# Kernel optimization log

Hardware: AMD Instinct MI355X
Metric: run time of the kernel (lower is better)

## Reference

```python
import jax, jax.numpy as jnp
import numpy as np
import math

# ---- static configuration (matches init_kwargs) ----
METADATA = [64, 48, 32]   # channels per l = 0,1,2
MAX_L = 3                 # order_out
N_BATCH = 32768
fact = math.factorial

def _cg_complex(l1, m1, l2, m2, l3, m3):
    # Clebsch-Gordan coefficient <l1 m1 l2 m2 | l3 m3> via Racah formula
    if m1 + m2 != m3 or l3 < abs(l1 - l2) or l3 > l1 + l2:
        return 0.0
    pre = math.sqrt((2*l3+1) * fact(l1+l2-l3) * fact(l1-l2+l3) * fact(-l1+l2+l3) / fact(l1+l2+l3+1))
    pre *= math.sqrt(fact(l1+m1)*fact(l1-m1)*fact(l2+m2)*fact(l2-m2)*fact(l3+m3)*fact(l3-m3))
    kmin = max(0, l2-l3-m1, l1-l3+m2)
    kmax = min(l1+l2-l3, l1-m1, l2+m2)
    s = 0.0
    for k in range(kmin, kmax+1):
        s += (-1)**k / (fact(k)*fact(l1+l2-l3-k)*fact(l1-m1-k)*fact(l2+m2-k)*fact(l3-l2+m1+k)*fact(l3-l1-m2+k))
    return pre * s

def _U(l):
    # complex->real spherical harmonic change of basis, rows = real m', cols = complex m
    U = np.zeros((2*l+1, 2*l+1), dtype=np.complex128)
    for m in range(-l, l+1):
        r = m + l
        if m > 0:
            U[r, m+l] = (-1)**m / math.sqrt(2.0); U[r, -m+l] = 1.0/math.sqrt(2.0)
        elif m == 0:
            U[r, l] = 1.0
        else:
            U[r, m+l] = 1j/math.sqrt(2.0); U[r, -m+l] = -1j*(-1)**m/math.sqrt(2.0)
    return U

def _real_cg(l1, l2, l3):
    Cc = np.zeros((2*l1+1, 2*l2+1, 2*l3+1))
    for m1 in range(-l1, l1+1):
        for m2 in range(-l2, l2+1):
            for m3 in range(-l3, l3+1):
                Cc[m1+l1, m2+l2, m3+l3] = _cg_complex(l1, m1, l2, m2, l3, m3)
    T = np.einsum('am,bn,co,mno->abc', _U(l1), _U(l2), _U(l3).conj(), Cc.astype(np.complex128))
    T = T.imag if np.abs(T.imag).max() > np.abs(T.real).max() else T.real
    return np.ascontiguousarray(T).astype(np.float32)

# ---- static index structures ----
L_IN = len(METADATA)
OFF_IN = np.concatenate([[0], np.cumsum([METADATA[l]*(2*l+1) for l in range(L_IN)])]).astype(np.int64)
DIM_IN = int(OFF_IN[-1])  # 368
PATHS = []
for l1 in range(L_IN):
    for l2 in range(L_IN):
        for l3 in range(abs(l1-l2), min(l1+l2, MAX_L)+1):
            PATHS.append((l1, l2, l3, min(METADATA[l1], METADATA[l2])))
MD_OV = [0]*(MAX_L+1)
for (_, _, l3, ch) in PATHS:
    MD_OV[l3] = max(MD_OV[l3], ch)
OFF_OUT = np.concatenate([[0], np.cumsum([MD_OV[l]*(2*l+1) for l in range(MAX_L+1)])]).astype(np.int64)
DIM_OUT = int(OFF_OUT[-1])  # 672
CG = {(l1, l2, l3): jnp.asarray(_real_cg(l1, l2, l3)) for (l1, l2, l3, _) in PATHS}

_mix_id, _scat = [], []
_base = 0
for (l1, l2, l3, ch) in PATHS:
    for i in range(ch):
        for m in range(2*l3+1):
            _mix_id.append(_base + i)
            _scat.append(int(OFF_OUT[l3]) + i*(2*l3+1) + m)
    _base += ch
MIX_ID = jnp.asarray(np.array(_mix_id, dtype=np.int64))
SCATTER = jnp.asarray(np.array(_scat, dtype=np.int64))
N_MIX = _base  # 688

_chan_in = []
_cb = 0
for l in range(L_IN):
    for i in range(METADATA[l]):
        _chan_in += [_cb + i]*(2*l+1)
    _cb += METADATA[l]
CHAN_IN = jnp.asarray(np.array(_chan_in, dtype=np.int64))
N_KEEP = _cb  # 144
_kin, _kout = [], []
for l in range(L_IN):
    cp = min(METADATA[l], MD_OV[l])
    for i in range(cp):
        for m in range(2*l+1):
            _kin.append(int(OFF_IN[l]) + i*(2*l+1) + m)
            _kout.append(int(OFF_OUT[l]) + i*(2*l+1) + m)
KEEP_IN = jnp.asarray(np.array(_kin, dtype=np.int64))
KEEP_OUT = jnp.asarray(np.array(_kout, dtype=np.int64))

SQ3 = math.sqrt(3.0)

def setup_inputs() -> dict:
    key = jax.random.key(0)
    k1, k2, k3 = jax.random.split(key, 3)
    x = jax.random.normal(k1, (N_BATCH, DIM_IN), dtype=jnp.float32)
    keep_coeff = jax.random.uniform(k2, (N_KEEP,), minval=-SQ3, maxval=SQ3, dtype=jnp.float32)
    mix_coeff = jax.random.uniform(k3, (N_MIX,), minval=-SQ3, maxval=SQ3, dtype=jnp.float32)
    return {"x": x, "keep_coeff": keep_coeff, "mix_coeff": mix_coeff}

def reference(x, keep_coeff, mix_coeff):
    n = x.shape[0]
    # keep path: per-channel coeff broadcast over m components
    x_keep = x * keep_coeff[CHAN_IN]  # [N, 368]
    # CG tensor-product self-coupling (diagonal channel pairing per path)
    tps = []
    for (l1, l2, l3, ch) in PATHS:
        x1 = x[:, OFF_IN[l1]:OFF_IN[l1]+ch*(2*l1+1)].reshape(n, ch, 2*l1+1)
        x2 = x[:, OFF_IN[l2]:OFF_IN[l2]+ch*(2*l2+1)].reshape(n, ch, 2*l2+1)
        tps.append(jnp.einsum('nia,nib,abm->nim', x1, x2, CG[(l1, l2, l3)]).reshape(n, -1))
    cat = jnp.concatenate(tps, axis=1)  # [N, 2576] non-overlapped TP output
    cat = cat * 0.5 * mix_coeff[MIX_ID]
    # scatter (index_add) into overlapped output layout
    out = jnp.zeros((n, DIM_OUT), dtype=x.dtype).at[:, SCATTER].add(cat)
    # gather + add of keep path (index_select + add_)
    out = out.at[:, KEEP_OUT].add(x_keep[:, KEEP_IN])
    return out
```

## Files before the change

kernel.cpp:

```cpp
#include <hip/hip_runtime.h>


namespace cgc {

struct cplx { double re, im; };
constexpr cplx cmul(cplx a, cplx b){ return {a.re*b.re - a.im*b.im, a.re*b.im + a.im*b.re}; }

constexpr double cfact(int n){ double r = 1.0; for (int i = 2; i <= n; ++i) r *= i; return r; }
constexpr double cabsd(double x){ return x < 0 ? -x : x; }

constexpr double csqrtd(double x){
  if (x <= 0.0) return 0.0;
  double g = x > 1.0 ? x : 1.0;
  for (int i = 0; i < 48; ++i) g = 0.5*(g + x/g);
  return g;
}

constexpr double SQRT2 = csqrtd(2.0);

constexpr double cg_complex(int l1,int m1,int l2,int m2,int l3,int m3){
  if (m1 + m2 != m3) return 0.0;
  int lo = l1 > l2 ? l1 - l2 : l2 - l1;
  if (l3 < lo || l3 > l1 + l2) return 0.0;
  double pre = csqrtd((2*l3+1) * cfact(l1+l2-l3)*cfact(l1-l2+l3)*cfact(-l1+l2+l3)/cfact(l1+l2+l3+1));
  pre *= csqrtd(cfact(l1+m1)*cfact(l1-m1)*cfact(l2+m2)*cfact(l2-m2)*cfact(l3+m3)*cfact(l3-m3));
  int kmin = 0;
  if (l2-l3-m1 > kmin) kmin = l2-l3-m1;
  if (l1-l3+m2 > kmin) kmin = l1-l3+m2;
  int kmax = l1+l2-l3;
  if (l1-m1 < kmax) kmax = l1-m1;
  if (l2+m2 < kmax) kmax = l2+m2;
  double s = 0.0;
  for (int k = kmin; k <= kmax; ++k){
    double d = cfact(k)*cfact(l1+l2-l3-k)*cfact(l1-m1-k)*cfact(l2+m2-k)
             * cfact(l3-l2+m1+k)*cfact(l3-l1-m2+k);
    s += ((k & 1) ? -1.0 : 1.0) / d;
  }
  return pre * s;
}

constexpr cplx Uent(int l, int r, int c){
  int m = r - l;
  if (m > 0){
    if (c ==  m + l) return { ((m & 1) ? -1.0 : 1.0)/SQRT2, 0.0 };
    if (c == -m + l) return { 1.0/SQRT2, 0.0 };
    return {0.0, 0.0};
  } else if (m == 0){
    if (c == l) return {1.0, 0.0};
    return {0.0, 0.0};
  } else {
    int ma = -m;
    if (c ==  m + l) return { 0.0, 1.0/SQRT2 };
    if (c == -m + l) return { 0.0, -(((ma & 1) ? -1.0 : 1.0))/SQRT2 };
    return {0.0, 0.0};
  }
}

template<int L1,int L2,int L3>
struct CGData { float w[(2*L1+1)*(2*L2+1)*(2*L3+1)]; };

template<int L1,int L2,int L3>
constexpr CGData<L1,L2,L3> make_cg(){
  constexpr int D1 = 2*L1+1, D2 = 2*L2+1, D3 = 2*L3+1;
  cplx U1[D1*D1] = {}; cplx U2[D2*D2] = {}; cplx U3c[D3*D3] = {};
  for (int r = 0; r < D1; ++r) for (int c = 0; c < D1; ++c) U1[r*D1+c] = Uent(L1, r, c);
  for (int r = 0; r < D2; ++r) for (int c = 0; c < D2; ++c) U2[r*D2+c] = Uent(L2, r, c);
  for (int r = 0; r < D3; ++r) for (int c = 0; c < D3; ++c){
    cplx u = Uent(L3, r, c); u.im = -u.im; U3c[r*D3+c] = u;
  }
  double Cc[D1*D2*D3] = {};
  for (int m1 = -L1; m1 <= L1; ++m1)
    for (int m2 = -L2; m2 <= L2; ++m2){
      int m3 = m1 + m2;
      if (m3 < -L3 || m3 > L3) continue;
      Cc[((m1+L1)*D2 + (m2+L2))*D3 + (m3+L3)] = cg_complex(L1,m1,L2,m2,L3,m3);
    }
  double re[D1*D2*D3] = {}; double im[D1*D2*D3] = {};
  for (int a = 0; a < D1; ++a)
    for (int b = 0; b < D2; ++b)
      for (int c = 0; c < D3; ++c){
        double sre = 0.0, sim = 0.0;
        for (int m = 0; m < D1; ++m)
          for (int n = 0; n < D2; ++n){
            int o = m + n - L1 - L2 + L3;
            if (o < 0 || o >= D3) continue;
            double cc = Cc[(m*D2+n)*D3 + o];
            if (cc == 0.0) continue;
            cplx p = cmul(cmul(U1[a*D1+m], U2[b*D2+n]), U3c[c*D3+o]);
            sre += p.re * cc; sim += p.im * cc;
          }
        re[(a*D2+b)*D3+c] = sre; im[(a*D2+b)*D3+c] = sim;
      }
  double mre = 0.0, mim = 0.0;
  for (int k = 0; k < D1*D2*D3; ++k){
    if (cabsd(re[k]) > mre) mre = cabsd(re[k]);
    if (cabsd(im[k]) > mim) mim = cabsd(im[k]);
  }
  CGData<L1,L2,L3> outv{};
  for (int k = 0; k < D1*D2*D3; ++k){
    double v = (mim > mre) ? im[k] : re[k];
    outv.w[k] = (cabsd(v) < 1e-10) ? 0.0f : (float)v;
  }
  return outv;
}

}

template<int L1,int L2,int L3>
__device__ __forceinline__ void tp_path(const float* xa, const float* xb, float cmix, float* acc){
  constexpr cgc::CGData<L1,L2,L3> cg = cgc::make_cg<L1,L2,L3>();
  constexpr int D1 = 2*L1+1, D2 = 2*L2+1, D3 = 2*L3+1;
  #pragma unroll
  for (int a = 0; a < D1; ++a){
    #pragma unroll
    for (int b = 0; b < D2; ++b){
      const float pr = xa[a] * xb[b];
      #pragma unroll
      for (int m = 0; m < D3; ++m){
        const float W = cg.w[(a*D2+b)*D3 + m];
        if (W != 0.0f) acc[m] += (cmix * W) * pr;
      }
    }
  }
}


__global__ __launch_bounds__(256) void selfmix_kernel(
    const float* __restrict__ x, const float* __restrict__ keep,
    const float* __restrict__ mix, float* __restrict__ out, int n)
{
  const long long gid = (long long)blockIdx.x * 256 + threadIdx.x;
  const long long nA = (long long)n * 32;
  const long long nB = (long long)n * 16;

  if (gid < nA){
    const int i   = (int)(gid & 31);
    const int row = (int)(gid >> 5);
    const float* xr = x + (long long)row * 368;
    float*     orow = out + (long long)row * 672;
    float s = xr[i];
    float p[3], d[5];
    #pragma unroll
    for (int k = 0; k < 3; ++k) p[k] = xr[64 + i*3 + k];
    #pragma unroll
    for (int k = 0; k < 5; ++k) d[k] = xr[208 + i*5 + k];

    float o0 = 0.f;
    float o1[3] = {0.f,0.f,0.f};
    float o2[5] = {0.f,0.f,0.f,0.f,0.f};
    float o3[7] = {0.f,0.f,0.f,0.f,0.f,0.f,0.f};

    tp_path<0,0,0>(&s,&s, 0.5f*mix[  0+i], &o0);
    tp_path<0,1,1>(&s, p, 0.5f*mix[ 64+i],  o1);
    tp_path<0,2,2>(&s, d, 0.5f*mix[112+i],  o2);
    tp_path<1,0,1>( p,&s, 0.5f*mix[144+i],  o1);
    tp_path<1,1,0>( p, p, 0.5f*mix[192+i], &o0);
    tp_path<1,1,1>( p, p, 0.5f*mix[240+i],  o1);
    tp_path<1,1,2>( p, p, 0.5f*mix[288+i],  o2);
    tp_path<1,2,1>( p, d, 0.5f*mix[336+i],  o1);
    tp_path<1,2,2>( p, d, 0.5f*mix[368+i],  o2);
    tp_path<1,2,3>( p, d, 0.5f*mix[400+i],  o3);
    tp_path<2,0,2>( d,&s, 0.5f*mix[432+i],  o2);
    tp_path<2,1,1>( d, p, 0.5f*mix[464+i],  o1);
    tp_path<2,1,2>( d, p, 0.5f*mix[496+i],  o2);
    tp_path<2,1,3>( d, p, 0.5f*mix[528+i],  o3);
    tp_path<2,2,0>( d, d, 0.5f*mix[560+i], &o0);
    tp_path<2,2,1>( d, d, 0.5f*mix[592+i],  o1);
    tp_path<2,2,2>( d, d, 0.5f*mix[624+i],  o2);
    tp_path<2,2,3>( d, d, 0.5f*mix[656+i],  o3);

    o0 += keep[i] * s;
    const float k1 = keep[64+i], k2 = keep[112+i];
    #pragma unroll
    for (int k = 0; k < 3; ++k) o1[k] += k1 * p[k];
    #pragma unroll
    for (int k = 0; k < 5; ++k) o2[k] += k2 * d[k];

    orow[i] = o0;
    #pragma unroll
    for (int k = 0; k < 3; ++k) orow[ 64 + i*3 + k] = o1[k];
    #pragma unroll
    for (int k = 0; k < 5; ++k) orow[208 + i*5 + k] = o2[k];
    #pragma unroll
    for (int k = 0; k < 7; ++k) orow[448 + i*7 + k] = o3[k];

  } else if (gid < nA + nB){
    const long long t = gid - nA;
    const int i   = 32 + (int)(t & 15);
    const int row = (int)(t >> 4);
    const float* xr = x + (long long)row * 368;
    float*     orow = out + (long long)row * 672;
    float s = xr[i];
    float p[3];
    #pragma unroll
    for (int k = 0; k < 3; ++k) p[k] = xr[64 + i*3 + k];

    float o0 = 0.f;
    float o1[3] = {0.f,0.f,0.f};
    float o2[5] = {0.f,0.f,0.f,0.f,0.f};

    tp_path<0,0,0>(&s,&s, 0.5f*mix[  0+i], &o0);
    tp_path<0,1,1>(&s, p, 0.5f*mix[ 64+i],  o1);
    tp_path<1,0,1>( p,&s, 0.5f*mix[144+i],  o1);
    tp_path<1,1,0>( p, p, 0.5f*mix[192+i], &o0);
    tp_path<1,1,1>( p, p, 0.5f*mix[240+i],  o1);
    tp_path<1,1,2>( p, p, 0.5f*mix[288+i],  o2);

    o0 += keep[i] * s;
    const float k1 = keep[64+i];
    #pragma unroll
    for (int k = 0; k < 3; ++k) o1[k] += k1 * p[k];

    orow[i] = o0;
    #pragma unroll
    for (int k = 0; k < 3; ++k) orow[ 64 + i*3 + k] = o1[k];
    #pragma unroll
    for (int k = 0; k < 5; ++k) orow[208 + i*5 + k] = o2[k];

  } else if (gid < nA + 2*nB){
    const long long t = gid - nA - nB;
    const int i   = 48 + (int)(t & 15);
    const int row = (int)(t >> 4);
    const float* xr = x + (long long)row * 368;
    float s = xr[i];
    float o0 = 0.f;
    tp_path<0,0,0>(&s,&s, 0.5f*mix[0+i], &o0);
    o0 += keep[i] * s;
    out[(long long)row * 672 + i] = o0;
  }
}

extern "C" void kernel_launch(void* const* d_in, const int* in_sizes, int n_in,
                              void* d_out, int out_size, void* d_ws, size_t ws_size,
                              hipStream_t stream)
{
  const float* x    = (const float*)d_in[0];
  const float* keep = (const float*)d_in[1];
  const float* mix  = (const float*)d_in[2];
  float* out = (float*)d_out;
  const int n = in_sizes[0] / 368;
  const long long total = (long long)n * 64;
  const int blocks = (int)((total + 255) / 256);
  selfmix_kernel<<<blocks, 256, 0, stream>>>(x, keep, mix, out, n);
}
```

Measured before the change: 136.8 us.

## Stage rows through shared memory for coalesced float4 loads and stores

Each block now handles four rows. It loads the input rows into shared memory with coalesced float4 reads, computes the tensor-product outputs into a padded shared output buffer, then writes the whole output rows back with coalesced float4 stores. This replaces strided per-thread global accesses (stride 3, 5, 7) with contiguous vector transfers. The costs are two block barriers, about 15 KB of shared memory per block, and an occupancy hint in the launch bounds.

Measured after the change: 149.4 us. 1.09x slower.

```diff
diff --git a/kernel.cpp b/kernel.cpp
--- a/kernel.cpp
+++ b/kernel.cpp
@@ -125,108 +125,139 @@
 }
 
 
-__global__ __launch_bounds__(256) void selfmix_kernel(
+constexpr int RPB      = 4;
+constexpr int IN_DIM   = 368;
+constexpr int OUT_DIM  = 672;
+constexpr int OUT_PAD  = 676;
+
+__global__ __launch_bounds__(256, 4) void selfmix_kernel(
     const float* __restrict__ x, const float* __restrict__ keep,
     const float* __restrict__ mix, float* __restrict__ out, int n)
 {
-  const long long gid = (long long)blockIdx.x * 256 + threadIdx.x;
-  const long long nA = (long long)n * 32;
-  const long long nB = (long long)n * 16;
-
-  if (gid < nA){
-    const int i   = (int)(gid & 31);
-    const int row = (int)(gid >> 5);
-    const float* xr = x + (long long)row * 368;
-    float*     orow = out + (long long)row * 672;
-    float s = xr[i];
-    float p[3], d[5];
-    #pragma unroll
-    for (int k = 0; k < 3; ++k) p[k] = xr[64 + i*3 + k];
-    #pragma unroll
-    for (int k = 0; k < 5; ++k) d[k] = xr[208 + i*5 + k];
-
-    float o0 = 0.f;
-    float o1[3] = {0.f,0.f,0.f};
-    float o2[5] = {0.f,0.f,0.f,0.f,0.f};
-    float o3[7] = {0.f,0.f,0.f,0.f,0.f,0.f,0.f};
-
-    tp_path<0,0,0>(&s,&s, 0.5f*mix[  0+i], &o0);
-    tp_path<0,1,1>(&s, p, 0.5f*mix[ 64+i],  o1);
-    tp_path<0,2,2>(&s, d, 0.5f*mix[112+i],  o2);
-    tp_path<1,0,1>( p,&s, 0.5f*mix[144+i],  o1);
-    tp_path<1,1,0>( p, p, 0.5f*mix[192+i], &o0);
-    tp_path<1,1,1>( p, p, 0.5f*mix[240+i],  o1);
-    tp_path<1,1,2>( p, p, 0.5f*mix[288+i],  o2);
-    tp_path<1,2,1>( p, d, 0.5f*mix[336+i],  o1);
-    tp_path<1,2,2>( p, d, 0.5f*mix[368+i],  o2);
-    tp_path<1,2,3>( p, d, 0.5f*mix[400+i],  o3);
-    tp_path<2,0,2>( d,&s, 0.5f*mix[432+i],  o2);
-    tp_path<2,1,1>( d, p, 0.5f*mix[464+i],  o1);
-    tp_path<2,1,2>( d, p, 0.5f*mix[496+i],  o2);
-    tp_path<2,1,3>( d, p, 0.5f*mix[528+i],  o3);
-    tp_path<2,2,0>( d, d, 0.5f*mix[560+i], &o0);
-    tp_path<2,2,1>( d, d, 0.5f*mix[592+i],  o1);
-    tp_path<2,2,2>( d, d, 0.5f*mix[624+i],  o2);
-    tp_path<2,2,3>( d, d, 0.5f*mix[656+i],  o3);
-
-    o0 += keep[i] * s;
-    const float k1 = keep[64+i], k2 = keep[112+i];
-    #pragma unroll
-    for (int k = 0; k < 3; ++k) o1[k] += k1 * p[k];
-    #pragma unroll
-    for (int k = 0; k < 5; ++k) o2[k] += k2 * d[k];
-
-    orow[i] = o0;
-    #pragma unroll
-    for (int k = 0; k < 3; ++k) orow[ 64 + i*3 + k] = o1[k];
-    #pragma unroll
-    for (int k = 0; k < 5; ++k) orow[208 + i*5 + k] = o2[k];
-    #pragma unroll
-    for (int k = 0; k < 7; ++k) orow[448 + i*7 + k] = o3[k];
-
-  } else if (gid < nA + nB){
-    const long long t = gid - nA;
-    const int i   = 32 + (int)(t & 15);
-    const int row = (int)(t >> 4);
-    const float* xr = x + (long long)row * 368;
-    float*     orow = out + (long long)row * 672;
-    float s = xr[i];
-    float p[3];
-    #pragma unroll
-    for (int k = 0; k < 3; ++k) p[k] = xr[64 + i*3 + k];
-
-    float o0 = 0.f;
-    float o1[3] = {0.f,0.f,0.f};
-    float o2[5] = {0.f,0.f,0.f,0.f,0.f};
-
-    tp_path<0,0,0>(&s,&s, 0.5f*mix[  0+i], &o0);
-    tp_path<0,1,1>(&s, p, 0.5f*mix[ 64+i],  o1);
-    tp_path<1,0,1>( p,&s, 0.5f*mix[144+i],  o1);
-    tp_path<1,1,0>( p, p, 0.5f*mix[192+i], &o0);
-    tp_path<1,1,1>( p, p, 0.5f*mix[240+i],  o1);
-    tp_path<1,1,2>( p, p, 0.5f*mix[288+i],  o2);
-
-    o0 += keep[i] * s;
-    const float k1 = keep[64+i];
-    #pragma unroll
-    for (int k = 0; k < 3; ++k) o1[k] += k1 * p[k];
-
-    orow[i] = o0;
-    #pragma unroll
-    for (int k = 0; k < 3; ++k) orow[ 64 + i*3 + k] = o1[k];
-    #pragma unroll
-    for (int k = 0; k < 5; ++k) orow[208 + i*5 + k] = o2[k];
-
-  } else if (gid < nA + 2*nB){
-    const long long t = gid - nA - nB;
-    const int i   = 48 + (int)(t & 15);
-    const int row = (int)(t >> 4);
-    const float* xr = x + (long long)row * 368;
-    float s = xr[i];
-    float o0 = 0.f;
-    tp_path<0,0,0>(&s,&s, 0.5f*mix[0+i], &o0);
-    o0 += keep[i] * s;
-    out[(long long)row * 672 + i] = o0;
+  __shared__ float sin_[RPB * IN_DIM];
+  __shared__ float sout[RPB * OUT_PAD];
+
+  const int tid  = threadIdx.x;
+  const int rb   = blockIdx.x * RPB;
+  const int rows = (n - rb < RPB) ? (n - rb) : RPB;
+
+  {
+    const float4* gx = (const float4*)(x + (size_t)rb * IN_DIM);
+    float4* s4 = (float4*)sin_;
+    const int nf4 = rows * (IN_DIM / 4);
+    for (int t = tid; t < nf4; t += 256) s4[t] = gx[t];
+  }
+  __syncthreads();
+
+  if (tid < 128){
+    const int row = tid >> 5;
+    const int i   = tid & 31;
+    if (row < rows){
+      const float* xr = sin_ + row * IN_DIM;
+      float*     orow = sout + row * OUT_PAD;
+      const float s = xr[i];
+      float p[3], d[5];
+      #pragma unroll
+      for (int k = 0; k < 3; ++k) p[k] = xr[64 + i*3 + k];
+      #pragma unroll
+      for (int k = 0; k < 5; ++k) d[k] = xr[208 + i*5 + k];
+
+      float o0 = 0.f;
+      float o1[3] = {0.f,0.f,0.f};
+      float o2[5] = {0.f,0.f,0.f,0.f,0.f};
+      float o3[7] = {0.f,0.f,0.f,0.f,0.f,0.f,0.f};
+
+      tp_path<0,0,0>(&s,&s, 0.5f*mix[  0+i], &o0);
+      tp_path<0,1,1>(&s, p, 0.5f*mix[ 64+i],  o1);
+      tp_path<0,2,2>(&s, d, 0.5f*mix[112+i],  o2);
+      tp_path<1,0,1>( p,&s, 0.5f*mix[144+i],  o1);
+      tp_path<1,1,0>( p, p, 0.5f*mix[192+i], &o0);
+      tp_path<1,1,1>( p, p, 0.5f*mix[240+i],  o1);
+      tp_path<1,1,2>( p, p, 0.5f*mix[288+i],  o2);
+      tp_path<1,2,1>( p, d, 0.5f*mix[336+i],  o1);
+      tp_path<1,2,2>( p, d, 0.5f*mix[368+i],  o2);
+      tp_path<1,2,3>( p, d, 0.5f*mix[400+i],  o3);
+      tp_path<2,0,2>( d,&s, 0.5f*mix[432+i],  o2);
+      tp_path<2,1,1>( d, p, 0.5f*mix[464+i],  o1);
+      tp_path<2,1,2>( d, p, 0.5f*mix[496+i],  o2);
+      tp_path<2,1,3>( d, p, 0.5f*mix[528+i],  o3);
+      tp_path<2,2,0>( d, d, 0.5f*mix[560+i], &o0);
+      tp_path<2,2,1>( d, d, 0.5f*mix[592+i],  o1);
+      tp_path<2,2,2>( d, d, 0.5f*mix[624+i],  o2);
+      tp_path<2,2,3>( d, d, 0.5f*mix[656+i],  o3);
+
+      o0 += keep[i] * s;
+      const float k1 = keep[64+i], k2 = keep[112+i];
+      #pragma unroll
+      for (int k = 0; k < 3; ++k) o1[k] += k1 * p[k];
+      #pragma unroll
+      for (int k = 0; k < 5; ++k) o2[k] += k2 * d[k];
+
+      orow[i] = o0;
+      #pragma unroll
+      for (int k = 0; k < 3; ++k) orow[ 64 + i*3 + k] = o1[k];
+      #pragma unroll
+      for (int k = 0; k < 5; ++k) orow[208 + i*5 + k] = o2[k];
+      #pragma unroll
+      for (int k = 0; k < 7; ++k) orow[448 + i*7 + k] = o3[k];
+    }
+  } else if (tid < 192){
+    const int u   = tid - 128;
+    const int row = u >> 4;
+    const int i   = 32 + (u & 15);
+    if (row < rows){
+      const float* xr = sin_ + row * IN_DIM;
+      float*     orow = sout + row * OUT_PAD;
+      const float s = xr[i];
+      float p[3];
+      #pragma unroll
+      for (int k = 0; k < 3; ++k) p[k] = xr[64 + i*3 + k];
+
+      float o0 = 0.f;
+      float o1[3] = {0.f,0.f,0.f};
+      float o2[5] = {0.f,0.f,0.f,0.f,0.f};
+
+      tp_path<0,0,0>(&s,&s, 0.5f*mix[  0+i], &o0);
+      tp_path<0,1,1>(&s, p, 0.5f*mix[ 64+i],  o1);
+      tp_path<1,0,1>( p,&s, 0.5f*mix[144+i],  o1);
+      tp_path<1,1,0>( p, p, 0.5f*mix[192+i], &o0);
+      tp_path<1,1,1>( p, p, 0.5f*mix[240+i],  o1);
+      tp_path<1,1,2>( p, p, 0.5f*mix[288+i],  o2);
+
+      o0 += keep[i] * s;
+      const float k1 = keep[64+i];
+      #pragma unroll
+      for (int k = 0; k < 3; ++k) o1[k] += k1 * p[k];
+
+      orow[i] = o0;
+      #pragma unroll
+      for (int k = 0; k < 3; ++k) orow[ 64 + i*3 + k] = o1[k];
+      #pragma unroll
+      for (int k = 0; k < 5; ++k) orow[208 + i*5 + k] = o2[k];
+    }
+  } else {
+    const int u   = tid - 192;
+    const int row = u >> 4;
+    const int i   = 48 + (u & 15);
+    if (row < rows){
+      const float s = sin_[row * IN_DIM + i];
+      float o0 = 0.f;
+      tp_path<0,0,0>(&s,&s, 0.5f*mix[0+i], &o0);
+      o0 += keep[i] * s;
+      sout[row * OUT_PAD + i] = o0;
+    }
+  }
+  __syncthreads();
+
+  {
+    float4* gout = (float4*)(out + (size_t)rb * OUT_DIM);
+    const float4* so4 = (const float4*)sout;
+    const int nf4 = rows * (OUT_DIM / 4);
+    for (int t = tid; t < nf4; t += 256){
+      const int r = t / 168;
+      const int j = t - r * 168;
+      gout[t] = so4[r * 169 + j];
+    }
   }
 }
 
@@ -238,8 +269,7 @@
   const float* keep = (const float*)d_in[1];
   const float* mix  = (const float*)d_in[2];
   float* out = (float*)d_out;
-  const int n = in_sizes[0] / 368;
-  const long long total = (long long)n * 64;
-  const int blocks = (int)((total + 255) / 256);
+  const int n = in_sizes[0] / IN_DIM;
+  const int blocks = (n + RPB - 1) / RPB;
   selfmix_kernel<<<blocks, 256, 0, stream>>>(x, keep, mix, out, n);
 }
```
